# Performance work log

Hardware: AMD Instinct MI355X
Metric: run time of the kernel (lower is better)

The kernel has to match this reference:

```python
import jax, jax.numpy as jnp
import numpy as np

EMB = 384
HEAD_DIM = 64  # emb_size / num_head = 384 / 6
B, S = 8, 2048


def setup_inputs() -> dict:
    key = jax.random.key(0)
    k1, k2, k3, k4 = jax.random.split(key, 4)
    x = jax.random.normal(k1, (B, S, EMB), dtype=jnp.float32)
    # nn.Linear(emb, head_dim, bias=False): store as [in, out] so q = x @ W
    scale = 0.02
    Wq = jax.random.normal(k2, (EMB, HEAD_DIM), dtype=jnp.float32) * scale
    Wk = jax.random.normal(k3, (EMB, HEAD_DIM), dtype=jnp.float32) * scale
    Wv = jax.random.normal(k4, (EMB, HEAD_DIM), dtype=jnp.float32) * scale
    return {"x": x, "Wq": Wq, "Wk": Wk, "Wv": Wv}


def reference(x, Wq, Wk, Wv):
    # x: [B, S, C]
    q = jnp.einsum('bsc,cd->bsd', x, Wq)  # [B,S,D]
    k = jnp.einsum('bsc,cd->bsd', x, Wk)
    v = jnp.einsum('bsc,cd->bsd', x, Wv)
    scores = jnp.einsum('bid,bjd->bij', q, k) * (HEAD_DIM ** -0.5)  # [B,S,S]
    # causal mask: positions with tril==0 (j > i) set to -inf
    causal = jnp.tril(jnp.ones((S, S), dtype=bool))  # [S,S]
    scores = jnp.where(causal[None, :, :], scores, -jnp.inf)
    # NOTE: faithful to original — softmax over dim=1 (query axis), not -1.
    attn = jax.nn.softmax(scores, axis=1)  # [B,S,S]
    out = jnp.einsum('bij,bjd->bid', attn, v)  # [B,S,D]
    return out
```

## Files before the change

kernel.cpp:

```cpp
#include <hip/hip_runtime.h>
#include <hip/hip_bf16.h>
#include <math.h>

#define B_N 8
#define S_N 2048
#define C_N 384
#define D_N 64
#define NEG_BIG (-1e30f)

typedef __bf16 bf16x8 __attribute__((ext_vector_type(8)));
typedef float f32x4 __attribute__((ext_vector_type(4)));

static __device__ __forceinline__ bf16x8 ldfrag(const __bf16* p) {
  return *reinterpret_cast<const bf16x8*>(p);
}

static __device__ __forceinline__ void gload16(void* lds, const void* gsrc) {
  __builtin_amdgcn_global_load_lds(
      (const __attribute__((address_space(1))) unsigned int*)gsrc,
      (__attribute__((address_space(3))) unsigned int*)lds, 16, 0, 0);
}

__global__ __launch_bounds__(256) void w_prep(
    const float* __restrict__ Wq, const float* __restrict__ Wk,
    const float* __restrict__ Wv, __bf16* __restrict__ Wt) {
  const int idx = blockIdx.x * 256 + threadIdx.x;
  const int m = idx / (64 * C_N);
  const int r = idx % (64 * C_N);
  const int d = r / C_N;
  const int c = r % C_N;
  const float* W = (m == 0) ? Wq : (m == 1) ? Wk : Wv;
  Wt[idx] = (__bf16)W[c * 64 + d];
}

__global__ __launch_bounds__(384) void qkv_mfma(
    const float* __restrict__ x, const __bf16* __restrict__ Wt,
    __bf16* __restrict__ Q, __bf16* __restrict__ K, __bf16* __restrict__ Vt) {
  const int t = threadIdx.x;
  const int w = t >> 6, lane = t & 63, lr = lane & 15, lg = lane >> 4;
  const int mat = w >> 1, rh = w & 1;
  const int row0 = blockIdx.x * 32;
  const int ri = row0 + rh * 16 + lr;

  __shared__ __bf16 vtile[32][66];

  const float scl = (mat == 0) ? 0.125f : 1.0f;
  const float* xr = x + (size_t)ri * C_N;
  const __bf16* Wm = Wt + (size_t)mat * 64 * C_N;

  f32x4 acc[4];
#pragma unroll
  for (int nt = 0; nt < 4; ++nt) acc[nt] = {0.f, 0.f, 0.f, 0.f};

  float4 xa = *reinterpret_cast<const float4*>(xr + lg * 8);
  float4 xb = *reinterpret_cast<const float4*>(xr + lg * 8 + 4);
  bf16x8 bw[4];
#pragma unroll
  for (int nt = 0; nt < 4; ++nt)
    bw[nt] = ldfrag(Wm + (size_t)(nt * 16 + lr) * C_N + lg * 8);

  for (int kk = 0; kk < C_N / 32; ++kk) {
    const int kn = (kk + 1 < C_N / 32) ? kk + 1 : kk;
    const float4 xan = *reinterpret_cast<const float4*>(xr + kn * 32 + lg * 8);
    const float4 xbn = *reinterpret_cast<const float4*>(xr + kn * 32 + lg * 8 + 4);
    bf16x8 bwn[4];
#pragma unroll
    for (int nt = 0; nt < 4; ++nt)
      bwn[nt] = ldfrag(Wm + (size_t)(nt * 16 + lr) * C_N + kn * 32 + lg * 8);

    bf16x8 a;
    a[0] = (__bf16)(xa.x * scl); a[1] = (__bf16)(xa.y * scl);
    a[2] = (__bf16)(xa.z * scl); a[3] = (__bf16)(xa.w * scl);
    a[4] = (__bf16)(xb.x * scl); a[5] = (__bf16)(xb.y * scl);
    a[6] = (__bf16)(xb.z * scl); a[7] = (__bf16)(xb.w * scl);
#pragma unroll
    for (int nt = 0; nt < 4; ++nt)
      acc[nt] = __builtin_amdgcn_mfma_f32_16x16x32_bf16(a, bw[nt], acc[nt], 0, 0, 0);

    xa = xan; xb = xbn;
#pragma unroll
    for (int nt = 0; nt < 4; ++nt) bw[nt] = bwn[nt];
  }

  if (mat < 2) {
    __bf16* outp = (mat == 0) ? Q : K;
#pragma unroll
    for (int nt = 0; nt < 4; ++nt)
#pragma unroll
      for (int r = 0; r < 4; ++r)
        outp[(size_t)(row0 + rh * 16 + lg * 4 + r) * 64 + nt * 16 + lr] =
            (__bf16)acc[nt][r];
  } else {
#pragma unroll
    for (int nt = 0; nt < 4; ++nt)
#pragma unroll
      for (int r = 0; r < 4; ++r)
        vtile[rh * 16 + lg * 4 + r][nt * 16 + lr] = (__bf16)acc[nt][r];
  }
  __syncthreads();

  const int b = row0 >> 11, s0 = row0 & (S_N - 1);
  for (int idx = t; idx < 64 * 32; idx += 384) {
    const int d = idx >> 5, s2 = idx & 31;
    Vt[((size_t)b * D_N + d) * S_N + s0 + s2] = vtile[s2][d];
  }
}

__global__ __launch_bounds__(1024) void col_stats(
    const __bf16* __restrict__ Q, const __bf16* __restrict__ K,
    float* __restrict__ zpart) {
  const int wg = blockIdx.x;
  const int b  = wg & 7;
  const int jb = (wg >> 3) & 31;
  const int h  = wg >> 8;
  const int j0 = jb * 64;

  const int t = threadIdx.x;
  const int w = t >> 6;
  const int s = w & 3;
  const int q = w >> 2;
  const int lane = t & 63, lr = lane & 15, lg = lane >> 4;

  const int n = 32 - jb;
  const int itStart = (h == 0) ? jb : jb + (n + 1) / 2;
  const int itEnd   = (h == 0) ? jb + (n + 1) / 2 : 32;
  float* zout = zpart + (size_t)h * B_N * S_N + (size_t)b * S_N;

  __shared__ __align__(16) __bf16 QT[2][64][64];
  __shared__ float zs[4][4][16];

  if (itStart >= itEnd) {
    if (w == 0 && lg == 0) {
      for (int c = lr; c < 64; c += 16) zout[j0 + c] = 0.f;
    }
    return;
  }

  const __bf16* Qb = Q + (size_t)b * S_N * 64;
  const __bf16* Kb = K + (size_t)b * S_N * 64;

  const int krow = j0 + q * 16 + lr;
  const bf16x8 bk0 = ldfrag(Kb + (size_t)krow * 64 + lg * 8);
  const bf16x8 bk1 = ldfrag(Kb + (size_t)krow * 64 + 32 + lg * 8);

  const int str  = t & 511;
  const int srow = str >> 3;
  const int schk = str & 7;
  const int gchk = schk ^ (srow & 7);
  const bool stager = (t < 512);

  if (stager)
    gload16(&QT[0][srow][schk * 8],
            Qb + (size_t)(itStart * 64 + srow) * 64 + gchk * 8);
  __syncthreads();

  float z = 0.f;
  int cur = 0;
  for (int it = itStart; it < itEnd; ++it) {
    const int i0 = it * 64;
    if (it + 1 < itEnd && stager)
      gload16(&QT[cur ^ 1][srow][schk * 8],
              Qb + (size_t)(i0 + 64 + srow) * 64 + gchk * 8);

    const int arow = s * 16 + lr;
    const bf16x8 aq0 = ldfrag(&QT[cur][arow][(lg ^ (arow & 7)) * 8]);
    const bf16x8 aq1 = ldfrag(&QT[cur][arow][((4 + lg) ^ (arow & 7)) * 8]);

    f32x4 s4 = {0.f, 0.f, 0.f, 0.f};
    s4 = __builtin_amdgcn_mfma_f32_16x16x32_bf16(aq0, bk0, s4, 0, 0, 0);
    s4 = __builtin_amdgcn_mfma_f32_16x16x32_bf16(aq1, bk1, s4, 0, 0, 0);

    const int ibase = i0 + s * 16 + lg * 4;
    const int jg = j0 + q * 16 + lr;
    if (it == jb) {
#pragma unroll
      for (int r = 0; r < 4; ++r)
        if (ibase + r < jg) s4[r] = NEG_BIG;
    }
    float es = __expf(s4[0]) + __expf(s4[1]) + __expf(s4[2]) + __expf(s4[3]);
    es += __shfl_xor(es, 16);
    es += __shfl_xor(es, 32);
    z += es;

    __syncthreads();
    cur ^= 1;
  }

  if (lg == 0) zs[s][q][lr] = z;
  __syncthreads();
  if (s == 0 && lg == 0) {
    const float zt = zs[0][q][lr] + zs[1][q][lr] + zs[2][q][lr] + zs[3][q][lr];
    zout[j0 + q * 16 + lr] = zt;
  }
}

__global__ __launch_bounds__(1024) void attn_out(
    const __bf16* __restrict__ Q, const __bf16* __restrict__ K,
    const __bf16* __restrict__ Vt, const float* __restrict__ zpart,
    float* __restrict__ opart) {
  const int wg = blockIdx.x;
  const int b  = wg & 7;
  const int ib = (wg >> 3) & 31;
  const int h  = wg >> 8;

  const int t = threadIdx.x;
  const int w = t >> 6;
  const int s = w & 3;
  const int q = w >> 2;
  const int lane = t & 63, lr = lane & 15, lg = lane >> 4;
  const int i0 = ib * 64;

  const int n = ib + 1;
  const int jbStart = (h == 0) ? 0 : (n + 1) / 2;
  const int jbEnd   = (h == 0) ? (n + 1) / 2 : n;

  float* op = opart + (size_t)h * B_N * S_N * D_N + (size_t)b * S_N * D_N;

  if (jbStart >= jbEnd) {
#pragma unroll
    for (int r = 0; r < 4; ++r)
      op[(size_t)(i0 + s * 16 + lg * 4 + r) * 64 + q * 16 + lr] = 0.f;
    return;
  }

  __shared__ __align__(16) __bf16 KT[2][64][64];
  __shared__ __align__(16) __bf16 VT[2][64][64];
  __shared__ __align__(16) __bf16 P[4][16][72];

  const __bf16* Qb  = Q  + (size_t)b * S_N * 64;
  const __bf16* Kb  = K  + (size_t)b * S_N * 64;
  const __bf16* Vtb = Vt + (size_t)b * D_N * S_N;
  const float*  zp0 = zpart + (size_t)b * S_N;
  const float*  zp1 = zpart + (size_t)B_N * S_N + (size_t)b * S_N;

  const int str  = t & 511;
  const int srow = str >> 3;
  const int schk = str & 7;
  const int gchk = schk ^ (srow & 7);
  const bool isK = (t < 512);

  const int ri = i0 + s * 16 + lr;
  const bf16x8 aq0 = ldfrag(Qb + (size_t)ri * 64 + lg * 8);
  const bf16x8 aq1 = ldfrag(Qb + (size_t)ri * 64 + 32 + lg * 8);
  const int ibase = i0 + s * 16 + lg * 4;

  f32x4 o = {0.f, 0.f, 0.f, 0.f};

  if (isK) gload16(&KT[0][srow][schk * 8],
                   Kb + (size_t)(jbStart * 64 + srow) * 64 + gchk * 8);
  else     gload16(&VT[0][srow][schk * 8],
                   Vtb + (size_t)srow * S_N + jbStart * 64 + gchk * 8);
  __syncthreads();

  int cur = 0;
  for (int jb = jbStart; jb < jbEnd; ++jb) {
    const int j0 = jb * 64;
    if (jb + 1 < jbEnd) {
      const int j0n = j0 + 64;
      if (isK) gload16(&KT[cur ^ 1][srow][schk * 8],
                       Kb + (size_t)(j0n + srow) * 64 + gchk * 8);
      else     gload16(&VT[cur ^ 1][srow][schk * 8],
                       Vtb + (size_t)srow * S_N + j0n + gchk * 8);
    }

    const int krow = q * 16 + lr;
    const bf16x8 bk0 = ldfrag(&KT[cur][krow][(lg ^ (krow & 7)) * 8]);
    const bf16x8 bk1 = ldfrag(&KT[cur][krow][((4 + lg) ^ (krow & 7)) * 8]);
    f32x4 s4 = {0.f, 0.f, 0.f, 0.f};
    s4 = __builtin_amdgcn_mfma_f32_16x16x32_bf16(aq0, bk0, s4, 0, 0, 0);
    s4 = __builtin_amdgcn_mfma_f32_16x16x32_bf16(aq1, bk1, s4, 0, 0, 0);

    const int jg = j0 + q * 16 + lr;
    const float rz = 1.0f / (zp0[jg] + zp1[jg]);
#pragma unroll
    for (int r = 0; r < 4; ++r) {
      const float pv = (jg <= ibase + r) ? __expf(s4[r]) * rz : 0.f;
      P[s][lg * 4 + r][q * 16 + lr] = (__bf16)pv;
    }
    __syncthreads();

    const bf16x8 ap0 = ldfrag(&P[s][lr][lg * 8]);
    const bf16x8 ap1 = ldfrag(&P[s][lr][32 + lg * 8]);
    const int vrow = q * 16 + lr;
    const bf16x8 bv0 = ldfrag(&VT[cur][vrow][(lg ^ (vrow & 7)) * 8]);
    const bf16x8 bv1 = ldfrag(&VT[cur][vrow][((4 + lg) ^ (vrow & 7)) * 8]);
    o = __builtin_amdgcn_mfma_f32_16x16x32_bf16(ap0, bv0, o, 0, 0, 0);
    o = __builtin_amdgcn_mfma_f32_16x16x32_bf16(ap1, bv1, o, 0, 0, 0);
    __syncthreads();
    cur ^= 1;
  }

#pragma unroll
  for (int r = 0; r < 4; ++r)
    op[(size_t)(i0 + s * 16 + lg * 4 + r) * 64 + q * 16 + lr] = o[r];
}

__global__ __launch_bounds__(256) void combine(
    const float* __restrict__ opart, float* __restrict__ out) {
  const size_t idx = (size_t)blockIdx.x * 256 + threadIdx.x;
  out[idx] = opart[idx] + opart[(size_t)B_N * S_N * D_N + idx];
}

extern "C" void kernel_launch(void* const* d_in, const int* in_sizes, int n_in,
                              void* d_out, int out_size, void* d_ws, size_t ws_size,
                              hipStream_t stream) {
  (void)in_sizes; (void)n_in; (void)ws_size; (void)out_size;
  const float* x  = (const float*)d_in[0];
  const float* Wq = (const float*)d_in[1];
  const float* Wk = (const float*)d_in[2];
  const float* Wv = (const float*)d_in[3];
  float* out = (float*)d_out;

  __bf16* Qb = (__bf16*)d_ws;
  __bf16* Kb = Qb + (size_t)B_N * S_N * D_N;
  __bf16* Vt = Kb + (size_t)B_N * S_N * D_N;
  float* zpart = (float*)(Vt + (size_t)B_N * S_N * D_N);
  float* opart = zpart + (size_t)2 * B_N * S_N;
  __bf16* Wt = (__bf16*)(opart + (size_t)2 * B_N * S_N * D_N);

  w_prep<<<dim3(3 * 64 * C_N / 256), dim3(256), 0, stream>>>(Wq, Wk, Wv, Wt);
  qkv_mfma<<<dim3(B_N * S_N / 32), dim3(384), 0, stream>>>(x, Wt, Qb, Kb, Vt);
  col_stats<<<dim3(2 * 32 * B_N), dim3(1024), 0, stream>>>(Qb, Kb, zpart);
  attn_out<<<dim3(2 * 32 * B_N), dim3(1024), 0, stream>>>(Qb, Kb, Vt, zpart, opart);
  combine<<<dim3(B_N * S_N * D_N / 256), dim3(256), 0, stream>>>(opart, out);
}
```

Before: 76.96 us.

## Split attention work four ways with smaller workgroups computing full tiles per wave

Raises the partition count for the column-stat and output kernels from two to four and shrinks workgroups from 1024 to 256 threads. Each wave now loops over four 16-wide subtiles inside a 64x64 tile instead of one wave per subtile, which removes the cross-wave LDS reduction of column sums and one barrier per iteration in attn_out. The aim is better load balance over the causal triangle and more independent workgroups per CU. The cost is more partial buffers for zpart and opart, extra global traffic in combine and in the normalizer reads, and fewer waves sharing each staged tile.

Measured after the change: 74.24 us (median of 2 runs). 1.04x faster.

```diff
diff --git a/kernel.cpp b/kernel.cpp
--- a/kernel.cpp
+++ b/kernel.cpp
@@ -6,6 +6,7 @@
 #define S_N 2048
 #define C_N 384
 #define D_N 64
+#define NPART 4
 #define NEG_BIG (-1e30f)
 
 typedef __bf16 bf16x8 __attribute__((ext_vector_type(8)));
@@ -106,7 +107,7 @@
   }
 }
 
-__global__ __launch_bounds__(1024) void col_stats(
+__global__ __launch_bounds__(256) void col_stats(
     const __bf16* __restrict__ Q, const __bf16* __restrict__ K,
     float* __restrict__ zpart) {
   const int wg = blockIdx.x;
@@ -116,25 +117,20 @@
   const int j0 = jb * 64;
 
   const int t = threadIdx.x;
-  const int w = t >> 6;
-  const int s = w & 3;
-  const int q = w >> 2;
+  const int q = t >> 6;
   const int lane = t & 63, lr = lane & 15, lg = lane >> 4;
 
   const int n = 32 - jb;
-  const int itStart = (h == 0) ? jb : jb + (n + 1) / 2;
-  const int itEnd   = (h == 0) ? jb + (n + 1) / 2 : 32;
+  const int itStart = jb + (n * h) / NPART;
+  const int itEnd   = jb + (n * (h + 1)) / NPART;
   float* zout = zpart + (size_t)h * B_N * S_N + (size_t)b * S_N;
 
+  if (itStart >= itEnd) {
+    if (lg == 0) zout[j0 + q * 16 + lr] = 0.f;
+    return;
+  }
+
   __shared__ __align__(16) __bf16 QT[2][64][64];
-  __shared__ float zs[4][4][16];
-
-  if (itStart >= itEnd) {
-    if (w == 0 && lg == 0) {
-      for (int c = lr; c < 64; c += 16) zout[j0 + c] = 0.f;
-    }
-    return;
-  }
 
   const __bf16* Qb = Q + (size_t)b * S_N * 64;
   const __bf16* Kb = K + (size_t)b * S_N * 64;
@@ -143,58 +139,54 @@
   const bf16x8 bk0 = ldfrag(Kb + (size_t)krow * 64 + lg * 8);
   const bf16x8 bk1 = ldfrag(Kb + (size_t)krow * 64 + 32 + lg * 8);
 
-  const int str  = t & 511;
-  const int srow = str >> 3;
-  const int schk = str & 7;
-  const int gchk = schk ^ (srow & 7);
-  const bool stager = (t < 512);
-
-  if (stager)
-    gload16(&QT[0][srow][schk * 8],
-            Qb + (size_t)(itStart * 64 + srow) * 64 + gchk * 8);
+  const int r0 = t >> 3, c0 = t & 7;
+  const int gq = c0 ^ (r0 & 7);
+
+#define STAGE_Q(BUF, TILE) do { \
+    gload16(&QT[BUF][r0][c0 * 8], Qb + (size_t)((TILE) * 64 + r0) * 64 + gq * 8); \
+    gload16(&QT[BUF][r0 + 32][c0 * 8], \
+            Qb + (size_t)((TILE) * 64 + r0 + 32) * 64 + gq * 8); \
+  } while (0)
+
+  STAGE_Q(0, itStart);
   __syncthreads();
 
   float z = 0.f;
   int cur = 0;
   for (int it = itStart; it < itEnd; ++it) {
     const int i0 = it * 64;
-    if (it + 1 < itEnd && stager)
-      gload16(&QT[cur ^ 1][srow][schk * 8],
-              Qb + (size_t)(i0 + 64 + srow) * 64 + gchk * 8);
-
-    const int arow = s * 16 + lr;
-    const bf16x8 aq0 = ldfrag(&QT[cur][arow][(lg ^ (arow & 7)) * 8]);
-    const bf16x8 aq1 = ldfrag(&QT[cur][arow][((4 + lg) ^ (arow & 7)) * 8]);
-
-    f32x4 s4 = {0.f, 0.f, 0.f, 0.f};
-    s4 = __builtin_amdgcn_mfma_f32_16x16x32_bf16(aq0, bk0, s4, 0, 0, 0);
-    s4 = __builtin_amdgcn_mfma_f32_16x16x32_bf16(aq1, bk1, s4, 0, 0, 0);
-
-    const int ibase = i0 + s * 16 + lg * 4;
-    const int jg = j0 + q * 16 + lr;
-    if (it == jb) {
-#pragma unroll
-      for (int r = 0; r < 4; ++r)
-        if (ibase + r < jg) s4[r] = NEG_BIG;
+    if (it + 1 < itEnd) STAGE_Q(cur ^ 1, it + 1);
+
+#pragma unroll
+    for (int s = 0; s < 4; ++s) {
+      const int arow = s * 16 + lr;
+      const bf16x8 aq0 = ldfrag(&QT[cur][arow][(lg ^ (arow & 7)) * 8]);
+      const bf16x8 aq1 = ldfrag(&QT[cur][arow][((4 + lg) ^ (arow & 7)) * 8]);
+      f32x4 s4 = {0.f, 0.f, 0.f, 0.f};
+      s4 = __builtin_amdgcn_mfma_f32_16x16x32_bf16(aq0, bk0, s4, 0, 0, 0);
+      s4 = __builtin_amdgcn_mfma_f32_16x16x32_bf16(aq1, bk1, s4, 0, 0, 0);
+      const int ibase = i0 + s * 16 + lg * 4;
+      const int jg = j0 + q * 16 + lr;
+      if (it == jb) {
+#pragma unroll
+        for (int r = 0; r < 4; ++r)
+          if (ibase + r < jg) s4[r] = NEG_BIG;
+      }
+      float es = __expf(s4[0]) + __expf(s4[1]) + __expf(s4[2]) + __expf(s4[3]);
+      es += __shfl_xor(es, 16);
+      es += __shfl_xor(es, 32);
+      z += es;
     }
-    float es = __expf(s4[0]) + __expf(s4[1]) + __expf(s4[2]) + __expf(s4[3]);
-    es += __shfl_xor(es, 16);
-    es += __shfl_xor(es, 32);
-    z += es;
 
     __syncthreads();
     cur ^= 1;
   }
-
-  if (lg == 0) zs[s][q][lr] = z;
-  __syncthreads();
-  if (s == 0 && lg == 0) {
-    const float zt = zs[0][q][lr] + zs[1][q][lr] + zs[2][q][lr] + zs[3][q][lr];
-    zout[j0 + q * 16 + lr] = zt;
-  }
-}
-
-__global__ __launch_bounds__(1024) void attn_out(
+#undef STAGE_Q
+
+  if (lg == 0) zout[j0 + q * 16 + lr] = z;
+}
+
+__global__ __launch_bounds__(256) void attn_out(
     const __bf16* __restrict__ Q, const __bf16* __restrict__ K,
     const __bf16* __restrict__ Vt, const float* __restrict__ zpart,
     float* __restrict__ opart) {
@@ -204,101 +196,104 @@
   const int h  = wg >> 8;
 
   const int t = threadIdx.x;
-  const int w = t >> 6;
-  const int s = w & 3;
-  const int q = w >> 2;
+  const int s = t >> 6;
   const int lane = t & 63, lr = lane & 15, lg = lane >> 4;
   const int i0 = ib * 64;
 
   const int n = ib + 1;
-  const int jbStart = (h == 0) ? 0 : (n + 1) / 2;
-  const int jbEnd   = (h == 0) ? (n + 1) / 2 : n;
+  const int jbStart = (n * h) / NPART;
+  const int jbEnd   = (n * (h + 1)) / NPART;
 
   float* op = opart + (size_t)h * B_N * S_N * D_N + (size_t)b * S_N * D_N;
-
-  if (jbStart >= jbEnd) {
+  const int ibase = i0 + s * 16 + lg * 4;
+
+  f32x4 o[4];
+#pragma unroll
+  for (int dt = 0; dt < 4; ++dt) o[dt] = {0.f, 0.f, 0.f, 0.f};
+
+  if (jbStart < jbEnd) {
+    __shared__ __align__(16) __bf16 KT[2][64][64];
+    __shared__ __align__(16) __bf16 VT[2][64][64];
+    __shared__ __align__(16) __bf16 P[4][16][72];
+
+    const __bf16* Qb  = Q  + (size_t)b * S_N * 64;
+    const __bf16* Kb  = K  + (size_t)b * S_N * 64;
+    const __bf16* Vtb = Vt + (size_t)b * D_N * S_N;
+    const float*  zp  = zpart + (size_t)b * S_N;
+
+    const int r0 = t >> 3, c0 = t & 7;
+    const int gq = c0 ^ (r0 & 7);
+
+#define STAGE_KV(BUF, TJ0) do { \
+      gload16(&KT[BUF][r0][c0 * 8], Kb + (size_t)((TJ0) + r0) * 64 + gq * 8); \
+      gload16(&KT[BUF][r0 + 32][c0 * 8], \
+              Kb + (size_t)((TJ0) + r0 + 32) * 64 + gq * 8); \
+      gload16(&VT[BUF][r0][c0 * 8], Vtb + (size_t)r0 * S_N + (TJ0) + gq * 8); \
+      gload16(&VT[BUF][r0 + 32][c0 * 8], \
+              Vtb + (size_t)(r0 + 32) * S_N + (TJ0) + gq * 8); \
+    } while (0)
+
+    const int ri = i0 + s * 16 + lr;
+    const bf16x8 aq0 = ldfrag(Qb + (size_t)ri * 64 + lg * 8);
+    const bf16x8 aq1 = ldfrag(Qb + (size_t)ri * 64 + 32 + lg * 8);
+
+    STAGE_KV(0, jbStart * 64);
+    __syncthreads();
+
+    int cur = 0;
+    for (int jb = jbStart; jb < jbEnd; ++jb) {
+      const int j0 = jb * 64;
+      if (jb + 1 < jbEnd) STAGE_KV(cur ^ 1, j0 + 64);
+
+#pragma unroll
+      for (int jt = 0; jt < 4; ++jt) {
+        const int krow = jt * 16 + lr;
+        const bf16x8 bk0 = ldfrag(&KT[cur][krow][(lg ^ (krow & 7)) * 8]);
+        const bf16x8 bk1 = ldfrag(&KT[cur][krow][((4 + lg) ^ (krow & 7)) * 8]);
+        f32x4 s4 = {0.f, 0.f, 0.f, 0.f};
+        s4 = __builtin_amdgcn_mfma_f32_16x16x32_bf16(aq0, bk0, s4, 0, 0, 0);
+        s4 = __builtin_amdgcn_mfma_f32_16x16x32_bf16(aq1, bk1, s4, 0, 0, 0);
+        const int jg = j0 + jt * 16 + lr;
+        const float rz = 1.0f / (zp[jg] + zp[(size_t)B_N * S_N + jg] +
+                                 zp[(size_t)2 * B_N * S_N + jg] +
+                                 zp[(size_t)3 * B_N * S_N + jg]);
+#pragma unroll
+        for (int r = 0; r < 4; ++r) {
+          const float pv = (jg <= ibase + r) ? __expf(s4[r]) * rz : 0.f;
+          P[s][lg * 4 + r][jt * 16 + lr] = (__bf16)pv;
+        }
+      }
+
+      const bf16x8 ap0 = ldfrag(&P[s][lr][lg * 8]);
+      const bf16x8 ap1 = ldfrag(&P[s][lr][32 + lg * 8]);
+#pragma unroll
+      for (int dt = 0; dt < 4; ++dt) {
+        const int vrow = dt * 16 + lr;
+        const bf16x8 bv0 = ldfrag(&VT[cur][vrow][(lg ^ (vrow & 7)) * 8]);
+        const bf16x8 bv1 = ldfrag(&VT[cur][vrow][((4 + lg) ^ (vrow & 7)) * 8]);
+        o[dt] = __builtin_amdgcn_mfma_f32_16x16x32_bf16(ap0, bv0, o[dt], 0, 0, 0);
+        o[dt] = __builtin_amdgcn_mfma_f32_16x16x32_bf16(ap1, bv1, o[dt], 0, 0, 0);
+      }
+
+      __syncthreads();
+      cur ^= 1;
+    }
+#undef STAGE_KV
+  }
+
+#pragma unroll
+  for (int dt = 0; dt < 4; ++dt)
 #pragma unroll
     for (int r = 0; r < 4; ++r)
-      op[(size_t)(i0 + s * 16 + lg * 4 + r) * 64 + q * 16 + lr] = 0.f;
-    return;
-  }
-
-  __shared__ __align__(16) __bf16 KT[2][64][64];
-  __shared__ __align__(16) __bf16 VT[2][64][64];
-  __shared__ __align__(16) __bf16 P[4][16][72];
-
-  const __bf16* Qb  = Q  + (size_t)b * S_N * 64;
-  const __bf16* Kb  = K  + (size_t)b * S_N * 64;
-  const __bf16* Vtb = Vt + (size_t)b * D_N * S_N;
-  const float*  zp0 = zpart + (size_t)b * S_N;
-  const float*  zp1 = zpart + (size_t)B_N * S_N + (size_t)b * S_N;
-
-  const int str  = t & 511;
-  const int srow = str >> 3;
-  const int schk = str & 7;
-  const int gchk = schk ^ (srow & 7);
-  const bool isK = (t < 512);
-
-  const int ri = i0 + s * 16 + lr;
-  const bf16x8 aq0 = ldfrag(Qb + (size_t)ri * 64 + lg * 8);
-  const bf16x8 aq1 = ldfrag(Qb + (size_t)ri * 64 + 32 + lg * 8);
-  const int ibase = i0 + s * 16 + lg * 4;
-
-  f32x4 o = {0.f, 0.f, 0.f, 0.f};
-
-  if (isK) gload16(&KT[0][srow][schk * 8],
-                   Kb + (size_t)(jbStart * 64 + srow) * 64 + gchk * 8);
-  else     gload16(&VT[0][srow][schk * 8],
-                   Vtb + (size_t)srow * S_N + jbStart * 64 + gchk * 8);
-  __syncthreads();
-
-  int cur = 0;
-  for (int jb = jbStart; jb < jbEnd; ++jb) {
-    const int j0 = jb * 64;
-    if (jb + 1 < jbEnd) {
-      const int j0n = j0 + 64;
-      if (isK) gload16(&KT[cur ^ 1][srow][schk * 8],
-                       Kb + (size_t)(j0n + srow) * 64 + gchk * 8);
-      else     gload16(&VT[cur ^ 1][srow][schk * 8],
-                       Vtb + (size_t)srow * S_N + j0n + gchk * 8);
-    }
-
-    const int krow = q * 16 + lr;
-    const bf16x8 bk0 = ldfrag(&KT[cur][krow][(lg ^ (krow & 7)) * 8]);
-    const bf16x8 bk1 = ldfrag(&KT[cur][krow][((4 + lg) ^ (krow & 7)) * 8]);
-    f32x4 s4 = {0.f, 0.f, 0.f, 0.f};
-    s4 = __builtin_amdgcn_mfma_f32_16x16x32_bf16(aq0, bk0, s4, 0, 0, 0);
-    s4 = __builtin_amdgcn_mfma_f32_16x16x32_bf16(aq1, bk1, s4, 0, 0, 0);
-
-    const int jg = j0 + q * 16 + lr;
-    const float rz = 1.0f / (zp0[jg] + zp1[jg]);
-#pragma unroll
-    for (int r = 0; r < 4; ++r) {
-      const float pv = (jg <= ibase + r) ? __expf(s4[r]) * rz : 0.f;
-      P[s][lg * 4 + r][q * 16 + lr] = (__bf16)pv;
-    }
-    __syncthreads();
-
-    const bf16x8 ap0 = ldfrag(&P[s][lr][lg * 8]);
-    const bf16x8 ap1 = ldfrag(&P[s][lr][32 + lg * 8]);
-    const int vrow = q * 16 + lr;
-    const bf16x8 bv0 = ldfrag(&VT[cur][vrow][(lg ^ (vrow & 7)) * 8]);
-    const bf16x8 bv1 = ldfrag(&VT[cur][vrow][((4 + lg) ^ (vrow & 7)) * 8]);
-    o = __builtin_amdgcn_mfma_f32_16x16x32_bf16(ap0, bv0, o, 0, 0, 0);
-    o = __builtin_amdgcn_mfma_f32_16x16x32_bf16(ap1, bv1, o, 0, 0, 0);
-    __syncthreads();
-    cur ^= 1;
-  }
-
-#pragma unroll
-  for (int r = 0; r < 4; ++r)
-    op[(size_t)(i0 + s * 16 + lg * 4 + r) * 64 + q * 16 + lr] = o[r];
+      op[(size_t)(ibase + r) * D_N + dt * 16 + lr] = o[dt][r];
 }
 
 __global__ __launch_bounds__(256) void combine(
     const float* __restrict__ opart, float* __restrict__ out) {
   const size_t idx = (size_t)blockIdx.x * 256 + threadIdx.x;
-  out[idx] = opart[idx] + opart[(size_t)B_N * S_N * D_N + idx];
+  const size_t stride = (size_t)B_N * S_N * D_N;
+  out[idx] = opart[idx] + opart[stride + idx] + opart[2 * stride + idx] +
+             opart[3 * stride + idx];
 }
 
 extern "C" void kernel_launch(void* const* d_in, const int* in_sizes, int n_in,
@@ -315,12 +310,12 @@
   __bf16* Kb = Qb + (size_t)B_N * S_N * D_N;
   __bf16* Vt = Kb + (size_t)B_N * S_N * D_N;
   float* zpart = (float*)(Vt + (size_t)B_N * S_N * D_N);
-  float* opart = zpart + (size_t)2 * B_N * S_N;
-  __bf16* Wt = (__bf16*)(opart + (size_t)2 * B_N * S_N * D_N);
+  float* opart = zpart + (size_t)NPART * B_N * S_N;
+  __bf16* Wt = (__bf16*)(opart + (size_t)NPART * B_N * S_N * D_N);
 
   w_prep<<<dim3(3 * 64 * C_N / 256), dim3(256), 0, stream>>>(Wq, Wk, Wv, Wt);
   qkv_mfma<<<dim3(B_N * S_N / 32), dim3(384), 0, stream>>>(x, Wt, Qb, Kb, Vt);
-  col_stats<<<dim3(2 * 32 * B_N), dim3(1024), 0, stream>>>(Qb, Kb, zpart);
-  attn_out<<<dim3(2 * 32 * B_N), dim3(1024), 0, stream>>>(Qb, Kb, Vt, zpart, opart);
+  col_stats<<<dim3(NPART * 32 * B_N), dim3(256), 0, stream>>>(Qb, Kb, zpart);
+  attn_out<<<dim3(NPART * 32 * B_N), dim3(256), 0, stream>>>(Qb, Kb, Vt, zpart, opart);
   combine<<<dim3(B_N * S_N * D_N / 256), dim3(256), 0, stream>>>(opart, out);
 }
```
